# Kernel optimization log

Hardware: AMD Instinct MI355X
Metric: run time of the kernel (lower is better)

Reference implementation:

```python
import jax, jax.numpy as jnp
import numpy as np

D_MODEL = 1024
N_HEADS = 16
D_FF = 4096
EPS = 1e-6


def layernorm(x, alpha, bias):
    # torch.std uses Bessel correction (ddof=1)
    mean = jnp.mean(x, axis=-1, keepdims=True)
    std = jnp.std(x, axis=-1, keepdims=True, ddof=1)
    return alpha * (x - mean) / (std + EPS) + bias


def setup_inputs() -> dict:
    key = jax.random.key(0)
    ks = jax.random.split(key, 12)
    s = 1.0 / np.sqrt(D_MODEL)
    sf = 1.0 / np.sqrt(D_FF)
    return {
        "x": jax.random.normal(ks[0], (2, 2048, D_MODEL), jnp.float32),
        "mask": jnp.ones((2, 1, 1, 2048), jnp.int32),
        "wq": jax.random.normal(ks[1], (D_MODEL, D_MODEL), jnp.float32) * s,
        "wk": jax.random.normal(ks[2], (D_MODEL, D_MODEL), jnp.float32) * s,
        "wv": jax.random.normal(ks[3], (D_MODEL, D_MODEL), jnp.float32) * s,
        "wo": jax.random.normal(ks[4], (D_MODEL, D_MODEL), jnp.float32) * s,
        "wo_b": jnp.zeros((D_MODEL,), jnp.float32),
        "w1": jax.random.normal(ks[5], (D_MODEL, D_FF), jnp.float32) * s,
        "b1": jnp.zeros((D_FF,), jnp.float32),
        "w2": jax.random.normal(ks[6], (D_FF, D_MODEL), jnp.float32) * sf,
        "b2": jnp.zeros((D_MODEL,), jnp.float32),
        "alpha1": jnp.ones((D_MODEL,), jnp.float32),
        "bias1": jnp.zeros((D_MODEL,), jnp.float32),
        "alpha2": jnp.ones((D_MODEL,), jnp.float32),
        "bias2": jnp.zeros((D_MODEL,), jnp.float32),
    }


def reference(x, mask, wq, wk, wv, wo, wo_b, w1, b1, w2, b2,
              alpha1, bias1, alpha2, bias2):
    B, S, D = x.shape
    h, dk = N_HEADS, D_MODEL // N_HEADS
    # projections -> [B, h, S, dk]
    q = (x @ wq).reshape(B, S, h, dk).transpose(0, 2, 1, 3)
    k = (x @ wk).reshape(B, S, h, dk).transpose(0, 2, 1, 3)
    v = (x @ wv).reshape(B, S, h, dk).transpose(0, 2, 1, 3)
    scores = jnp.einsum('bhqd,bhkd->bhqk', q, k) / jnp.sqrt(jnp.float32(dk))
    scores = jnp.where(mask == 0, jnp.float32(-1e9), scores)
    attn = jax.nn.softmax(scores, axis=-1)
    ctx = jnp.einsum('bhqk,bhkd->bhqd', attn, v)
    ctx = ctx.transpose(0, 2, 1, 3).reshape(B, S, D)
    attn_out = ctx @ wo + wo_b
    x = layernorm(x + attn_out, alpha1, bias1)
    ff = jax.nn.relu(x @ w1 + b1) @ w2 + b2
    x = layernorm(x + ff, alpha2, bias2)
    return x
```

## Files before the change

kernel.cpp:

```cpp
#include <hip/hip_runtime.h>
#include <hip/hip_bf16.h>

#define D_MODEL 1024
#define N_HEADS 16
#define DK      64
#define SEQ     2048
#define BATCH   2
#define D_FF    4096
#define ROWS    (BATCH*SEQ)
#define LN_EPS  1e-6f
#define KTILE   128

typedef __hip_bfloat16 bf16;
typedef __attribute__((ext_vector_type(8))) short frag8;
typedef __attribute__((ext_vector_type(4))) float facc4;

__device__ inline float bf2f(unsigned short u){ return __uint_as_float(((unsigned)u) << 16); }
__device__ inline float toF(bf16 v){ return __bfloat162float(v); }
__device__ inline unsigned short f2bu(float f){ bf16 h = __float2bfloat16(f); return *reinterpret_cast<unsigned short*>(&h); }

__device__ inline float ld1(const void* p, size_t idx, bool f32) {
    return f32 ? ((const float*)p)[idx] : toF(((const bf16*)p)[idx]);
}

struct U8 { unsigned short v[8]; };
__device__ inline U8 ld8bf(const void* p, size_t idx, bool f32) {
    U8 r;
    if (!f32) {
        *reinterpret_cast<uint4*>(r.v) = *reinterpret_cast<const uint4*>((const unsigned short*)p + idx);
    } else {
        const float* f = (const float*)p + idx;
        const float4 a = *reinterpret_cast<const float4*>(f);
        const float4 b = *reinterpret_cast<const float4*>(f + 4);
        r.v[0]=f2bu(a.x); r.v[1]=f2bu(a.y); r.v[2]=f2bu(a.z); r.v[3]=f2bu(a.w);
        r.v[4]=f2bu(b.x); r.v[5]=f2bu(b.y); r.v[6]=f2bu(b.z); r.v[7]=f2bu(b.w);
    }
    return r;
}

__device__ inline void gld16(const void* g, void* l) {
    __builtin_amdgcn_global_load_lds(
        reinterpret_cast<const __attribute__((address_space(1))) void*>(
            reinterpret_cast<uintptr_t>(g)),
        reinterpret_cast<__attribute__((address_space(3))) void*>(
            (unsigned int)reinterpret_cast<uintptr_t>(l)),
        16, 0, 0);
}

__global__ void probe_kernel(const void* __restrict__ xp, int* __restrict__ flag) {
    __shared__ int hit;
    if (threadIdx.x == 0) hit = 0;
    __syncthreads();
    const bf16* p = (const bf16*)xp;
    int bad = 0;
    for (int i = threadIdx.x; i < 8192; i += 256) {
        float v = fabsf(toF(p[i]));
        if (!(v <= 1e5f)) bad = 1;
    }
    if (bad) atomicOr(&hit, 1);
    __syncthreads();
    if (threadIdx.x == 0) *flag = hit;
}

__global__ __launch_bounds__(256) void xcvt_kernel(const void* __restrict__ x,
    bf16* __restrict__ out, const int* __restrict__ flagp)
{
    const bool f32 = (*flagp) != 0;
    const size_t i = ((size_t)blockIdx.x * 256 + threadIdx.x) * 8;
    U8 d = ld8bf(x, i, f32);
    *reinterpret_cast<uint4*>(out + i) = *reinterpret_cast<const uint4*>(d.v);
}

__global__ __launch_bounds__(256) void transpose_kernel(const void* __restrict__ W,
    bf16* __restrict__ WT, int K, int N, const int* __restrict__ flagp)
{
    const bool f32 = (*flagp) != 0;
    __shared__ float tile[32][33];
    const int tx = threadIdx.x, ty = threadIdx.y;
    const int n0 = blockIdx.x * 32, k0 = blockIdx.y * 32;
    #pragma unroll
    for (int r = 0; r < 4; ++r)
        tile[ty + 8*r][tx] = ld1(W, (size_t)(k0 + ty + 8*r) * N + n0 + tx, f32);
    __syncthreads();
    #pragma unroll
    for (int r = 0; r < 4; ++r)
        WT[(size_t)(n0 + ty + 8*r) * K + k0 + tx] = __float2bfloat16(tile[tx][ty + 8*r]);
}

__global__ __launch_bounds__(256) void transpose4_kernel(const void* __restrict__ w0,
    const void* __restrict__ w1, const void* __restrict__ w2, const void* __restrict__ w3,
    bf16* __restrict__ WT4, const int* __restrict__ flagp)
{
    const bool f32 = (*flagp) != 0;
    const int which = blockIdx.z;
    const void* W = (which == 0) ? w0 : (which == 1) ? w1 : (which == 2) ? w2 : w3;
    bf16* WT = WT4 + (size_t)which * D_MODEL * D_MODEL;
    __shared__ float tile[32][33];
    const int tx = threadIdx.x, ty = threadIdx.y;
    const int n0 = blockIdx.x * 32, k0 = blockIdx.y * 32;
    #pragma unroll
    for (int r = 0; r < 4; ++r)
        tile[ty + 8*r][tx] = ld1(W, (size_t)(k0 + ty + 8*r) * D_MODEL + n0 + tx, f32);
    __syncthreads();
    #pragma unroll
    for (int r = 0; r < 4; ++r)
        WT[(size_t)(n0 + ty + 8*r) * D_MODEL + k0 + tx] = __float2bfloat16(tile[tx][ty + 8*r]);
}

__global__ __launch_bounds__(256) void vtrans_kernel(const bf16* __restrict__ V,
    bf16* __restrict__ VT)
{
    __shared__ unsigned short tile[32][33];
    const int tx = threadIdx.x, ty = threadIdx.y;
    const int s0 = blockIdx.x * 32, d0 = blockIdx.y * 32;
    const int bh = blockIdx.z, b = bh >> 4, h = bh & 15;
    #pragma unroll
    for (int r = 0; r < 4; ++r)
        tile[ty + 8*r][tx] = *reinterpret_cast<const unsigned short*>(
            V + ((size_t)(b * SEQ + s0 + ty + 8*r)) * D_MODEL + h * DK + d0 + tx);
    __syncthreads();
    #pragma unroll
    for (int r = 0; r < 4; ++r)
        *reinterpret_cast<unsigned short*>(
            VT + ((size_t)(bh * DK + d0 + ty + 8*r)) * SEQ + s0 + tx) = tile[tx][ty + 8*r];
}

template<bool RELU, bool BIAS, int NMAT, int SPLITK>
__global__ __launch_bounds__(256) void mgemm_kernel(const bf16* __restrict__ A,
    const bf16* __restrict__ BT, const void* __restrict__ bias,
    bf16* __restrict__ C, int M, int N, int K, const int* __restrict__ flagp)
{
    const bool inF32 = (*flagp) != 0;

    __shared__ unsigned short sA[128 * 64];
    __shared__ unsigned short sB[128 * 64];

    int which = 0, colb = blockIdx.x;
    if (NMAT > 1) { which = blockIdx.x >> 3; colb = blockIdx.x & 7; }
    const int kslice = (SPLITK > 1) ? blockIdx.z : 0;
    const int Kspan  = K / SPLITK;
    const int kbase  = kslice * Kspan;
    const bf16* Bp = BT + (size_t)which * N * K;
    bf16*       Cp = C  + (size_t)which * M * N + (size_t)kslice * M * N;

    const int row0 = blockIdx.y * 128;
    const int col0 = colb * 128;

    const int t    = threadIdx.x;
    const int wave = t >> 6;
    const int lane = t & 63;
    const int lm   = lane & 15;
    const int q    = lane >> 4;
    const int wm   = (wave & 1) * 64;
    const int wn   = (wave >> 1) * 64;

    facc4 acc[4][4];
    #pragma unroll
    for (int i = 0; i < 4; ++i)
        #pragma unroll
        for (int j = 0; j < 4; ++j)
            acc[i][j] = (facc4){0.f, 0.f, 0.f, 0.f};

    for (int k0 = kbase; k0 < kbase + Kspan; k0 += 64) {
        __syncthreads();
        #pragma unroll
        for (int j = 0; j < 4; ++j) {
            const int ch = (wave * 4 + j) * 64 + lane;
            const int r  = ch >> 3;
            const int cs = ch & 7;
            const int c  = cs ^ (r & 7);
            gld16(A  + (size_t)(row0 + r) * K + k0 + 8 * c, &sA[(wave * 4 + j) * 512]);
            gld16(Bp + (size_t)(col0 + r) * K + k0 + 8 * c, &sB[(wave * 4 + j) * 512]);
        }
        __syncthreads();

        #pragma unroll
        for (int kk = 0; kk < 64; kk += 32) {
            const int cr = (kk >> 3) + q;
            frag8 af[4], bfr[4];
            #pragma unroll
            for (int im = 0; im < 4; ++im) {
                const int m = wm + 16 * im + lm;
                af[im] = *reinterpret_cast<const frag8*>(&sA[m * 64 + ((cr ^ (m & 7)) << 3)]);
            }
            #pragma unroll
            for (int in = 0; in < 4; ++in) {
                const int n = wn + 16 * in + lm;
                bfr[in] = *reinterpret_cast<const frag8*>(&sB[n * 64 + ((cr ^ (n & 7)) << 3)]);
            }
            #pragma unroll
            for (int im = 0; im < 4; ++im)
                #pragma unroll
                for (int in = 0; in < 4; ++in)
                    acc[im][in] = __builtin_amdgcn_mfma_f32_16x16x32_bf16(af[im], bfr[in], acc[im][in], 0, 0, 0);
        }
    }

    #pragma unroll
    for (int in = 0; in < 4; ++in) {
        const int col = col0 + wn + 16*in + lm;
        float bv = 0.f;
        if (BIAS && kslice == 0) bv = ld1(bias, col, inF32);
        #pragma unroll
        for (int im = 0; im < 4; ++im) {
            #pragma unroll
            for (int r = 0; r < 4; ++r) {
                const int row = row0 + wm + 16*im + 4*q + r;
                float v = acc[im][in][r] + bv;
                if (RELU) v = fmaxf(v, 0.f);
                Cp[(size_t)row * N + col] = __float2bfloat16(v);
            }
        }
    }
}

__global__ __launch_bounds__(256, 2) void fattn_kernel(
    const bf16* __restrict__ Qg, const bf16* __restrict__ Kg,
    const bf16* __restrict__ VTg, const int* __restrict__ mask,
    bf16* __restrict__ ctx)
{
    __shared__ unsigned short sK[128 * 64];
    __shared__ unsigned short sV[64 * 128];
    __shared__ __align__(16) float madd[KTILE];

    const int t    = threadIdx.x;
    const int qt   = blockIdx.x;
    const int h    = blockIdx.y;
    const int b    = blockIdx.z;
    const int q0   = qt * 128;
    const int bh   = b * N_HEADS + h;
    const int wave = t >> 6;
    const int lane = t & 63;
    const int lm   = lane & 15;
    const int qd   = lane >> 4;
    const bool qo  = (qd & 1) != 0;

    frag8 qf[2][2];
    #pragma unroll
    for (int s = 0; s < 2; ++s) {
        const bf16* qsrc = Qg + ((size_t)(b * SEQ + q0 + 32 * wave + 16 * s + lm)) * D_MODEL + h * DK;
        qf[s][0] = *reinterpret_cast<const frag8*>(qsrc + 8 * qd);
        qf[s][1] = *reinterpret_cast<const frag8*>(qsrc + 32 + 8 * qd);
    }

    facc4 accO[2][4];
    #pragma unroll
    for (int s = 0; s < 2; ++s)
        #pragma unroll
        for (int in = 0; in < 4; ++in) accO[s][in] = (facc4){0.f, 0.f, 0.f, 0.f};
    float m_r[2] = {-1e30f, -1e30f}, l_r[2] = {0.f, 0.f};

    for (int kt = 0; kt < SEQ / KTILE; ++kt) {
        const int k0 = kt * KTILE;
        __syncthreads();

        #pragma unroll
        for (int j = 0; j < 4; ++j) {
            const int ch = (wave * 4 + j) * 64 + lane;
            const int rK = ch >> 3, cK = (ch & 7) ^ (rK & 7);
            gld16(Kg + ((size_t)(b * SEQ + k0 + rK)) * D_MODEL + h * DK + 8 * cK,
                  &sK[(wave * 4 + j) * 512]);
            const int rV = ch >> 4, cV = (ch & 15) ^ (rV & 15);
            gld16(VTg + ((size_t)(bh * DK + rV)) * SEQ + k0 + 8 * cV,
                  &sV[(wave * 4 + j) * 512]);
        }
        if (t < KTILE) madd[t] = (mask[b * SEQ + k0 + t] == 0) ? -1e9f : 0.f;
        __syncthreads();

        facc4 accST[2][8];
        #pragma unroll
        for (int s = 0; s < 2; ++s)
            #pragma unroll
            for (int i = 0; i < 8; ++i) accST[s][i] = (facc4){0.f, 0.f, 0.f, 0.f};
        #pragma unroll
        for (int i = 0; i < 8; ++i) {
            #pragma unroll
            for (int s2 = 0; s2 < 2; ++s2) {
                const int cr = 4 * s2 + qd;
                frag8 kf = *reinterpret_cast<const frag8*>(
                    &sK[(16 * i + lm) * 64 + ((cr ^ (lm & 7)) << 3)]);
                accST[0][i] = __builtin_amdgcn_mfma_f32_16x16x32_bf16(kf, qf[0][s2], accST[0][i], 0, 0, 0);
                accST[1][i] = __builtin_amdgcn_mfma_f32_16x16x32_bf16(kf, qf[1][s2], accST[1][i], 0, 0, 0);
            }
        }

        float m0[2] = {-1e30f, -1e30f};
        #pragma unroll
        for (int i = 0; i < 8; ++i) {
            const facc4 mv = *reinterpret_cast<const facc4*>(&madd[16 * i + 4 * qd]);
            #pragma unroll
            for (int s = 0; s < 2; ++s) {
                #pragma unroll
                for (int r = 0; r < 4; ++r) {
                    accST[s][i][r] = fmaf(accST[s][i][r], 0.125f, mv[r]);
                    m0[s] = fmaxf(m0[s], accST[s][i][r]);
                }
            }
        }
        float mn[2], alpha[2];
        #pragma unroll
        for (int s = 0; s < 2; ++s) {
            m0[s] = fmaxf(m0[s], __shfl_xor(m0[s], 16));
            m0[s] = fmaxf(m0[s], __shfl_xor(m0[s], 32));
            mn[s] = fmaxf(m_r[s], m0[s]);
            alpha[s] = __expf(m_r[s] - mn[s]);
            m_r[s] = mn[s];
        }

        unsigned up[2][8][2];
        float ps[2] = {0.f, 0.f};
        #pragma unroll
        for (int s = 0; s < 2; ++s) {
            #pragma unroll
            for (int i = 0; i < 8; ++i) {
                const float p0 = __expf(accST[s][i][0] - mn[s]);
                const float p1 = __expf(accST[s][i][1] - mn[s]);
                const float p2 = __expf(accST[s][i][2] - mn[s]);
                const float p3 = __expf(accST[s][i][3] - mn[s]);
                ps[s] += (p0 + p1) + (p2 + p3);
                up[s][i][0] = (unsigned)f2bu(p0) | ((unsigned)f2bu(p1) << 16);
                up[s][i][1] = (unsigned)f2bu(p2) | ((unsigned)f2bu(p3) << 16);
            }
        }
        #pragma unroll
        for (int s = 0; s < 2; ++s) {
            ps[s] += __shfl_xor(ps[s], 16);
            ps[s] += __shfl_xor(ps[s], 32);
            l_r[s] = l_r[s] * alpha[s] + ps[s];
            #pragma unroll
            for (int in = 0; in < 4; ++in)
                #pragma unroll
                for (int r = 0; r < 4; ++r) accO[s][in][r] *= alpha[s];
        }

        #pragma unroll
        for (int c = 0; c < 4; ++c) {
            union { frag8 f; unsigned u[4]; } pf0_, pf1_;
            #pragma unroll
            for (int s = 0; s < 2; ++s) {
                unsigned a0 = up[s][2*c][0],     a1 = up[s][2*c][1];
                unsigned b0 = up[s][2*c + 1][0], b1 = up[s][2*c + 1][1];
                asm("v_permlane32_swap_b32 %0, %1" : "+v"(a0), "+v"(b0));
                asm("v_permlane32_swap_b32 %0, %1" : "+v"(a1), "+v"(b1));
                const unsigned t0 = qo ? a0 : b0;
                const unsigned t1 = qo ? a1 : b1;
                const unsigned r0 = __shfl_xor(t0, 16);
                const unsigned r1 = __shfl_xor(t1, 16);
                unsigned u0 = qo ? r0 : a0;
                unsigned u1 = qo ? r1 : a1;
                unsigned u2 = qo ? b0 : r0;
                unsigned u3 = qo ? b1 : r1;
                if (s == 0) { pf0_.u[0]=u0; pf0_.u[1]=u1; pf0_.u[2]=u2; pf0_.u[3]=u3; }
                else        { pf1_.u[0]=u0; pf1_.u[1]=u1; pf1_.u[2]=u2; pf1_.u[3]=u3; }
            }
            #pragma unroll
            for (int in = 0; in < 4; ++in) {
                const int cr = 4 * c + qd;
                frag8 vf = *reinterpret_cast<const frag8*>(
                    &sV[(16 * in + lm) * 128 + ((cr ^ lm) << 3)]);
                accO[0][in] = __builtin_amdgcn_mfma_f32_16x16x32_bf16(vf, pf0_.f, accO[0][in], 0, 0, 0);
                accO[1][in] = __builtin_amdgcn_mfma_f32_16x16x32_bf16(vf, pf1_.f, accO[1][in], 0, 0, 0);
            }
        }
    }

    #pragma unroll
    for (int s = 0; s < 2; ++s) {
        const float invl = 1.f / l_r[s];
        bf16* crow = ctx + ((size_t)(b * SEQ + q0 + 32 * wave + 16 * s + lm)) * D_MODEL + h * DK;
        #pragma unroll
        for (int in = 0; in < 4; ++in) {
            union { uint2 v; unsigned short sh[4]; } ov;
            #pragma unroll
            for (int r = 0; r < 4; ++r) ov.sh[r] = f2bu(accO[s][in][r] * invl);
            *reinterpret_cast<uint2*>(crow + 16 * in + 4 * qd) = ov.v;
        }
    }
}

template<bool BASE_WS, bool OUT_WS>
__global__ __launch_bounds__(256) void ln_kernel(const void* __restrict__ base,
    const bf16* __restrict__ addv, const bf16* __restrict__ addv2,
    const void* __restrict__ alpha, const void* __restrict__ bias,
    void* __restrict__ outp, const int* __restrict__ flagp)
{
    const bool inF32 = (*flagp) != 0;
    __shared__ float vals[D_MODEL];
    __shared__ float red[256];
    const int row = blockIdx.x, tid = threadIdx.x;

    float lsum = 0.f;
    for (int i = tid; i < D_MODEL; i += 256) {
        const size_t off = (size_t)row * D_MODEL + i;
        float v = (BASE_WS ? toF(((const bf16*)base)[off]) : ld1(base, off, inF32)) + toF(addv[off]);
        if (addv2) v += toF(addv2[off]);
        vals[i] = v; lsum += v;
    }
    red[tid] = lsum; __syncthreads();
    for (int s = 128; s > 0; s >>= 1) { if (tid < s) red[tid] += red[tid + s]; __syncthreads(); }
    const float mean = red[0] / (float)D_MODEL; __syncthreads();

    float lsq = 0.f;
    for (int i = tid; i < D_MODEL; i += 256) { float dd = vals[i] - mean; lsq += dd * dd; }
    red[tid] = lsq; __syncthreads();
    for (int s = 128; s > 0; s >>= 1) { if (tid < s) red[tid] += red[tid + s]; __syncthreads(); }
    const float var = red[0] / (float)(D_MODEL - 1);
    const float inv = 1.f / (sqrtf(var) + LN_EPS);

    for (int i = tid; i < D_MODEL; i += 256) {
        const size_t off = (size_t)row * D_MODEL + i;
        const float y = ld1(alpha, i, inF32) * (vals[i] - mean) * inv + ld1(bias, i, inF32);
        if (OUT_WS || !inF32) ((bf16*)outp)[off] = __float2bfloat16(y);
        else                  ((float*)outp)[off] = y;
    }
}

extern "C" void kernel_launch(void* const* d_in, const int* in_sizes, int n_in,
                              void* d_out, int out_size, void* d_ws, size_t ws_size,
                              hipStream_t stream)
{
    const void* x    = d_in[0];
    const int*  mask = (const int*)d_in[1];
    const void* wq   = d_in[2];
    const void* wk   = d_in[3];
    const void* wv   = d_in[4];
    const void* wo   = d_in[5];
    const void* wo_b = d_in[6];
    const void* w1   = d_in[7];
    const void* b1   = d_in[8];
    const void* w2   = d_in[9];
    const void* b2   = d_in[10];
    const void* al1  = d_in[11];
    const void* bi1  = d_in[12];
    const void* al2  = d_in[13];
    const void* bi2  = d_in[14];

    const size_t MB = 1024 * 1024;
    char* ws = (char*)d_ws;
    const bool BIG = ws_size >= 64 * MB + 4096;
    if (!BIG && ws_size < 56 * MB + 4096) return;

    dim3 tb(32, 8);

    if (BIG) {
        bf16* Qb   = (bf16*)(ws + 0 * MB);
        bf16* Kb   = (bf16*)(ws + 8 * MB);
        bf16* Vb   = (bf16*)(ws + 16 * MB);
        bf16* Xb   = (bf16*)(ws + 24 * MB);
        bf16* VTb  = (bf16*)(ws + 24 * MB);
        bf16* WT4  = (bf16*)(ws + 32 * MB);
        bf16* WOT  = WT4 + (size_t)3 * D_MODEL * D_MODEL;
        bf16* W1T  = (bf16*)(ws + 40 * MB);
        bf16* W2T  = (bf16*)(ws + 48 * MB);
        bf16* CTXb = (bf16*)(ws + 56 * MB);
        bf16* ATT0 = (bf16*)(ws + 0 * MB);
        bf16* ATT1 = (bf16*)(ws + 8 * MB);
        bf16* X1b  = (bf16*)(ws + 56 * MB);
        bf16* FFb  = (bf16*)(ws + 0 * MB);
        bf16* X20  = (bf16*)(ws + 32 * MB);
        bf16* X21  = (bf16*)(ws + 40 * MB);
        int*  flagp = (int*)(ws + 64 * MB);

        probe_kernel<<<1, 256, 0, stream>>>(x, flagp);
        xcvt_kernel<<<dim3(ROWS * D_MODEL / 2048), 256, 0, stream>>>(x, Xb, flagp);

        transpose4_kernel<<<dim3(32, 32, 4), tb, 0, stream>>>(wq, wk, wv, wo, WT4, flagp);
        transpose_kernel<<<dim3(128, 32), tb, 0, stream>>>(w1, W1T, D_MODEL, D_FF, flagp);
        transpose_kernel<<<dim3(32, 128), tb, 0, stream>>>(w2, W2T, D_FF, D_MODEL, flagp);

        mgemm_kernel<false, false, 3, 1><<<dim3(24, 32), 256, 0, stream>>>(
            Xb, WT4, nullptr, Qb, ROWS, D_MODEL, D_MODEL, flagp);

        vtrans_kernel<<<dim3(SEQ / 32, 2, BATCH * N_HEADS), tb, 0, stream>>>(Vb, VTb);

        fattn_kernel<<<dim3(SEQ / 128, N_HEADS, BATCH), 256, 0, stream>>>(Qb, Kb, VTb, mask, CTXb);

        mgemm_kernel<false, true, 1, 2><<<dim3(8, 32, 2), 256, 0, stream>>>(
            CTXb, WOT, wo_b, ATT0, ROWS, D_MODEL, D_MODEL, flagp);
        ln_kernel<false, true><<<ROWS, 256, 0, stream>>>(x, ATT0, ATT1, al1, bi1, X1b, flagp);

        mgemm_kernel<true, true, 1, 1><<<dim3(32, 32), 256, 0, stream>>>(
            X1b, W1T, b1, FFb, ROWS, D_FF, D_MODEL, flagp);

        mgemm_kernel<false, true, 1, 2><<<dim3(8, 32, 2), 256, 0, stream>>>(
            FFb, W2T, b2, X20, ROWS, D_MODEL, D_FF, flagp);
        ln_kernel<true, false><<<ROWS, 256, 0, stream>>>(X1b, X20, X21, al2, bi2, d_out, flagp);
    } else {
        bf16* Qb    = (bf16*)(ws + 0 * MB);
        bf16* Kb    = (bf16*)(ws + 8 * MB);
        bf16* Vb    = (bf16*)(ws + 16 * MB);
        bf16* Xb    = (bf16*)(ws + 24 * MB);
        bf16* VTb   = (bf16*)(ws + 24 * MB);
        bf16* WQKVT = (bf16*)(ws + 32 * MB);
        bf16* CTXb  = (bf16*)(ws + 32 * MB);
        bf16* W2T   = (bf16*)(ws + 32 * MB);
        bf16* WOT   = (bf16*)(ws + 0 * MB);
        bf16* ATT0  = (bf16*)(ws + 48 * MB);
        bf16* W1T   = (bf16*)(ws + 48 * MB);
        bf16* X20   = (bf16*)(ws + 48 * MB);
        bf16* X1b   = (bf16*)(ws + 40 * MB);
        bf16* FFb   = (bf16*)(ws + 0 * MB);
        int*  flagp = (int*)(ws + 56 * MB);

        probe_kernel<<<1, 256, 0, stream>>>(x, flagp);
        xcvt_kernel<<<dim3(ROWS * D_MODEL / 2048), 256, 0, stream>>>(x, Xb, flagp);

        transpose_kernel<<<dim3(32, 32), tb, 0, stream>>>(wq, WQKVT,           D_MODEL, D_MODEL, flagp);
        transpose_kernel<<<dim3(32, 32), tb, 0, stream>>>(wk, WQKVT + 1048576, D_MODEL, D_MODEL, flagp);
        transpose_kernel<<<dim3(32, 32), tb, 0, stream>>>(wv, WQKVT + 2097152, D_MODEL, D_MODEL, flagp);

        mgemm_kernel<false, false, 3, 1><<<dim3(24, 32), 256, 0, stream>>>(
            Xb, WQKVT, nullptr, Qb, ROWS, D_MODEL, D_MODEL, flagp);

        vtrans_kernel<<<dim3(SEQ / 32, 2, BATCH * N_HEADS), tb, 0, stream>>>(Vb, VTb);

        fattn_kernel<<<dim3(SEQ / 128, N_HEADS, BATCH), 256, 0, stream>>>(Qb, Kb, VTb, mask, CTXb);

        transpose_kernel<<<dim3(32, 32), tb, 0, stream>>>(wo, WOT, D_MODEL, D_MODEL, flagp);
        mgemm_kernel<false, true, 1, 1><<<dim3(8, 32), 256, 0, stream>>>(
            CTXb, WOT, wo_b, ATT0, ROWS, D_MODEL, D_MODEL, flagp);
        ln_kernel<false, true><<<ROWS, 256, 0, stream>>>(x, ATT0, nullptr, al1, bi1, X1b, flagp);

        transpose_kernel<<<dim3(128, 32), tb, 0, stream>>>(w1, W1T, D_MODEL, D_FF, flagp);
        mgemm_kernel<true, true, 1, 1><<<dim3(32, 32), 256, 0, stream>>>(
            X1b, W1T, b1, FFb, ROWS, D_FF, D_MODEL, flagp);

        transpose_kernel<<<dim3(32, 128), tb, 0, stream>>>(w2, W2T, D_FF, D_MODEL, flagp);
        mgemm_kernel<false, true, 1, 1><<<dim3(8, 32), 256, 0, stream>>>(
            FFb, W2T, b2, X20, ROWS, D_MODEL, D_FF, flagp);
        ln_kernel<true, false><<<ROWS, 256, 0, stream>>>(X1b, X20, nullptr, al2, bi2, d_out, flagp);
    }
}
```

Measured before the change: 394.3 us.

## Double-buffer K/V tiles in flash attention, use exp2 and lazy rescaling

The attention kernel now double-buffers the K and V shared-memory tiles. The next tile's global-to-LDS loads are issued before computing on the current tile, which removes one barrier per iteration and overlaps load latency with MFMA work. The whole mask row is precomputed once into shared memory. The softmax folds log2(e) into the score scale so it can use native exp2, and it skips the rescaling of the output accumulator when the running max grows by less than a threshold. The changes roughly double LDS use, which may lower occupancy. Correctness depends on the async LDS loads being complete by the single remaining barrier.

```diff
diff --git a/kernel.cpp b/kernel.cpp
--- a/kernel.cpp
+++ b/kernel.cpp
@@ -219,9 +219,9 @@
     const bf16* __restrict__ VTg, const int* __restrict__ mask,
     bf16* __restrict__ ctx)
 {
-    __shared__ unsigned short sK[128 * 64];
-    __shared__ unsigned short sV[64 * 128];
-    __shared__ __align__(16) float madd[KTILE];
+    __shared__ unsigned short sK[2][128 * 64];
+    __shared__ unsigned short sV[2][64 * 128];
+    __shared__ __align__(16) float madd[SEQ];
 
     const int t    = threadIdx.x;
     const int qt   = blockIdx.x;
@@ -235,6 +235,29 @@
     const int qd   = lane >> 4;
     const bool qo  = (qd & 1) != 0;
 
+    const float SCL = 0.18033688011112042f;
+
+    auto stage = [&](int bi, int kt) {
+        const int k0 = kt * KTILE;
+        #pragma unroll
+        for (int j = 0; j < 4; ++j) {
+            const int ch = (wave * 4 + j) * 64 + lane;
+            const int rK = ch >> 3, cK = (ch & 7) ^ (rK & 7);
+            gld16(Kg + ((size_t)(b * SEQ + k0 + rK)) * D_MODEL + h * DK + 8 * cK,
+                  &sK[bi][(wave * 4 + j) * 512]);
+            const int rV = ch >> 4, cV = (ch & 15) ^ (rV & 15);
+            gld16(VTg + ((size_t)(bh * DK + rV)) * SEQ + k0 + 8 * cV,
+                  &sV[bi][(wave * 4 + j) * 512]);
+        }
+    };
+
+    stage(0, 0);
+    #pragma unroll
+    for (int i = 0; i < SEQ / 256; ++i) {
+        const int idx = i * 256 + t;
+        madd[idx] = (mask[b * SEQ + idx] == 0) ? -1.442695e9f : 0.f;
+    }
+
     frag8 qf[2][2];
     #pragma unroll
     for (int s = 0; s < 2; ++s) {
@@ -251,21 +274,10 @@
     float m_r[2] = {-1e30f, -1e30f}, l_r[2] = {0.f, 0.f};
 
     for (int kt = 0; kt < SEQ / KTILE; ++kt) {
-        const int k0 = kt * KTILE;
+        const int cur = kt & 1;
+        const int k0  = kt * KTILE;
         __syncthreads();
-
-        #pragma unroll
-        for (int j = 0; j < 4; ++j) {
-            const int ch = (wave * 4 + j) * 64 + lane;
-            const int rK = ch >> 3, cK = (ch & 7) ^ (rK & 7);
-            gld16(Kg + ((size_t)(b * SEQ + k0 + rK)) * D_MODEL + h * DK + 8 * cK,
-                  &sK[(wave * 4 + j) * 512]);
-            const int rV = ch >> 4, cV = (ch & 15) ^ (rV & 15);
-            gld16(VTg + ((size_t)(bh * DK + rV)) * SEQ + k0 + 8 * cV,
-                  &sV[(wave * 4 + j) * 512]);
-        }
-        if (t < KTILE) madd[t] = (mask[b * SEQ + k0 + t] == 0) ? -1e9f : 0.f;
-        __syncthreads();
+        if (kt + 1 < SEQ / KTILE) stage(cur ^ 1, kt + 1);
 
         facc4 accST[2][8];
         #pragma unroll
@@ -278,7 +290,7 @@
             for (int s2 = 0; s2 < 2; ++s2) {
                 const int cr = 4 * s2 + qd;
                 frag8 kf = *reinterpret_cast<const frag8*>(
-                    &sK[(16 * i + lm) * 64 + ((cr ^ (lm & 7)) << 3)]);
+                    &sK[cur][(16 * i + lm) * 64 + ((cr ^ (lm & 7)) << 3)]);
                 accST[0][i] = __builtin_amdgcn_mfma_f32_16x16x32_bf16(kf, qf[0][s2], accST[0][i], 0, 0, 0);
                 accST[1][i] = __builtin_amdgcn_mfma_f32_16x16x32_bf16(kf, qf[1][s2], accST[1][i], 0, 0, 0);
             }
@@ -287,24 +299,31 @@
         float m0[2] = {-1e30f, -1e30f};
         #pragma unroll
         for (int i = 0; i < 8; ++i) {
-            const facc4 mv = *reinterpret_cast<const facc4*>(&madd[16 * i + 4 * qd]);
+            const facc4 mv = *reinterpret_cast<const facc4*>(&madd[k0 + 16 * i + 4 * qd]);
             #pragma unroll
             for (int s = 0; s < 2; ++s) {
                 #pragma unroll
                 for (int r = 0; r < 4; ++r) {
-                    accST[s][i][r] = fmaf(accST[s][i][r], 0.125f, mv[r]);
+                    accST[s][i][r] = fmaf(accST[s][i][r], SCL, mv[r]);
                     m0[s] = fmaxf(m0[s], accST[s][i][r]);
                 }
             }
         }
-        float mn[2], alpha[2];
+        float mn[2], alpha[2] = {1.f, 1.f};
+        bool resc[2];
         #pragma unroll
         for (int s = 0; s < 2; ++s) {
             m0[s] = fmaxf(m0[s], __shfl_xor(m0[s], 16));
             m0[s] = fmaxf(m0[s], __shfl_xor(m0[s], 32));
-            mn[s] = fmaxf(m_r[s], m0[s]);
-            alpha[s] = __expf(m_r[s] - mn[s]);
-            m_r[s] = mn[s];
+            const bool skip = __all(m0[s] - m_r[s] <= 11.54f) != 0;
+            resc[s] = !skip;
+            if (skip) {
+                mn[s] = m_r[s];
+            } else {
+                mn[s] = fmaxf(m_r[s], m0[s]);
+                alpha[s] = __builtin_amdgcn_exp2f(m_r[s] - mn[s]);
+                m_r[s] = mn[s];
+            }
         }
 
         unsigned up[2][8][2];
@@ -313,10 +332,10 @@
         for (int s = 0; s < 2; ++s) {
             #pragma unroll
             for (int i = 0; i < 8; ++i) {
-                const float p0 = __expf(accST[s][i][0] - mn[s]);
-                const float p1 = __expf(accST[s][i][1] - mn[s]);
-                const float p2 = __expf(accST[s][i][2] - mn[s]);
-                const float p3 = __expf(accST[s][i][3] - mn[s]);
+                const float p0 = __builtin_amdgcn_exp2f(accST[s][i][0] - mn[s]);
+                const float p1 = __builtin_amdgcn_exp2f(accST[s][i][1] - mn[s]);
+                const float p2 = __builtin_amdgcn_exp2f(accST[s][i][2] - mn[s]);
+                const float p3 = __builtin_amdgcn_exp2f(accST[s][i][3] - mn[s]);
                 ps[s] += (p0 + p1) + (p2 + p3);
                 up[s][i][0] = (unsigned)f2bu(p0) | ((unsigned)f2bu(p1) << 16);
                 up[s][i][1] = (unsigned)f2bu(p2) | ((unsigned)f2bu(p3) << 16);
@@ -326,11 +345,15 @@
         for (int s = 0; s < 2; ++s) {
             ps[s] += __shfl_xor(ps[s], 16);
             ps[s] += __shfl_xor(ps[s], 32);
-            l_r[s] = l_r[s] * alpha[s] + ps[s];
-            #pragma unroll
-            for (int in = 0; in < 4; ++in)
+            if (resc[s]) {
+                l_r[s] = l_r[s] * alpha[s] + ps[s];
                 #pragma unroll
-                for (int r = 0; r < 4; ++r) accO[s][in][r] *= alpha[s];
+                for (int in = 0; in < 4; ++in)
+                    #pragma unroll
+                    for (int r = 0; r < 4; ++r) accO[s][in][r] *= alpha[s];
+            } else {
+                l_r[s] += ps[s];
+            }
         }
 
         #pragma unroll
@@ -357,7 +380,7 @@
             for (int in = 0; in < 4; ++in) {
                 const int cr = 4 * c + qd;
                 frag8 vf = *reinterpret_cast<const frag8*>(
-                    &sV[(16 * in + lm) * 128 + ((cr ^ lm) << 3)]);
+                    &sV[cur][(16 * in + lm) * 128 + ((cr ^ lm) << 3)]);
                 accO[0][in] = __builtin_amdgcn_mfma_f32_16x16x32_bf16(vf, pf0_.f, accO[0][in], 0, 0, 0);
                 accO[1][in] = __builtin_amdgcn_mfma_f32_16x16x32_bf16(vf, pf1_.f, accO[1][in], 0, 0, 0);
             }
```

Result: no change. 396.4 us (+0.5%).
